# Optimization experiments

Hardware: AMD Instinct MI355X
Metric: run time of the kernel (lower is better)

## Reference

```python
import jax, jax.numpy as jnp
import numpy as np

# Layer widths of the hardcoded torch MLP: 2->128->256->512->512->512->512->256->128->3
_DIMS = [2, 128, 256, 512, 512, 512, 512, 256, 128, 3]


def setup_inputs() -> dict:
    key = jax.random.key(0)
    keys = jax.random.split(key, 2 * (len(_DIMS) - 1) + 1)
    inp = {"x": jax.random.uniform(keys[0], (1048576, 2), dtype=jnp.float32)}
    for i in range(len(_DIMS) - 1):
        fan_in, fan_out = _DIMS[i], _DIMS[i + 1]
        bound = 1.0 / np.sqrt(fan_in)  # torch nn.Linear default init range
        inp[f"W{i+1}"] = jax.random.uniform(keys[2 * i + 1], (fan_in, fan_out), jnp.float32, -bound, bound)
        inp[f"b{i+1}"] = jax.random.uniform(keys[2 * i + 2], (fan_out,), jnp.float32, -bound, bound)
    return inp


def reference(x, W1, b1, W2, b2, W3, b3, W4, b4, W5, b5, W6, b6, W7, b7, W8, b8, W9, b9):
    # (transpose of torch's [out, in]); math is identical: y = x @ W + b.
    h = x
    for W, b in ((W1, b1), (W2, b2), (W3, b3), (W4, b4),
                 (W5, b5), (W6, b6), (W7, b7), (W8, b8)):
        h = jax.nn.relu(h @ W + b)
    return jax.nn.sigmoid(h @ W9 + b9)
```

## Files before the change

kernel.cpp:

```cpp
#include <hip/hip_runtime.h>

typedef _Float16 f16;
typedef __attribute__((ext_vector_type(4))) _Float16 f16x4;
typedef __attribute__((ext_vector_type(8))) _Float16 f16x8;
typedef __attribute__((ext_vector_type(16))) float f32x16;

#define MT 128
#define NBF 4
#define LDSP 1024
#define RING_B 32768

#define OFF2 0
#define OFF3 32768
#define OFF4 163840
#define OFF5 425984
#define OFF6 688128
#define OFF7 950272
#define OFF8 1081344
#define OFF9 1114112
#define TOTAL_FRAG_LANES 139776

__device__ __forceinline__ uint32_t swz(int row, int colbytes) {
  return (uint32_t)(row * LDSP + (colbytes ^ ((row & 31) << 4)));
}

__global__ void repack_kernel(const float* __restrict__ W2, const float* __restrict__ W3,
                              const float* __restrict__ W4, const float* __restrict__ W5,
                              const float* __restrict__ W6, const float* __restrict__ W7,
                              const float* __restrict__ W8, const float* __restrict__ W9,
                              f16* __restrict__ ws) {
  int gid = blockIdx.x * 256 + threadIdx.x;
  if (gid >= TOTAL_FRAG_LANES) return;
  const float* src; int N, NT; size_t dst; int local;
  if      (gid <   4096) { src = W2; N = 256; NT = 8;  dst = OFF2; local = gid;          }
  else if (gid <  20480) { src = W3; N = 512; NT = 16; dst = OFF3; local = gid -   4096; }
  else if (gid <  53248) { src = W4; N = 512; NT = 16; dst = OFF4; local = gid -  20480; }
  else if (gid <  86016) { src = W5; N = 512; NT = 16; dst = OFF5; local = gid -  53248; }
  else if (gid < 118784) { src = W6; N = 512; NT = 16; dst = OFF6; local = gid -  86016; }
  else if (gid < 135168) { src = W7; N = 256; NT = 8;  dst = OFF7; local = gid - 118784; }
  else if (gid < 139264) { src = W8; N = 128; NT = 4;  dst = OFF8; local = gid - 135168; }
  else                   { src = W9; N = 3;   NT = 1;  dst = OFF9; local = gid - 139264; }
  int lane = local & 63;
  int frag = local >> 6;
  int kf = frag / NT, nf = frag % NT;
  int n  = nf * 32 + (lane & 31);
  int kb = kf * 16 + ((lane >> 5) << 3);
  f16x8 v;
  #pragma unroll
  for (int i = 0; i < 8; ++i) {
    float val = (n < N) ? src[(size_t)(kb + i) * N + n] : 0.0f;
    v[i] = (f16)val;
  }
  *reinterpret_cast<f16x8*>(ws + dst + (size_t)local * 8) = v;
}

__device__ __forceinline__ void gload16(const f16* g, char* l) {
  __builtin_amdgcn_global_load_lds(
      (const __attribute__((address_space(1))) void*)g,
      (__attribute__((address_space(3))) void*)l, 16, 0, 0);
}

template<int MF>
__device__ __forceinline__ void stage_step(const f16* __restrict__ wp, int t,
                                           char* ringwave, int wid, int lane) {
  constexpr int KPS = 16 / MF;
  char* dst = ringwave + ((t & 1) << 11);
  int g0, g1;
  if constexpr (MF == 16) { g0 = t * 16 + wid * 2;       g1 = g0 + 1; }
  else                    { g0 = (t * KPS) * MF + wid;   g1 = (t * KPS + 1) * MF + wid; }
  gload16(wp + (size_t)g0 * 512 + (size_t)lane * 8, dst);
  gload16(wp + (size_t)g1 * 512 + (size_t)lane * 8, dst + 1024);
}

template<int KT, int MF, int NXT_MF, bool STAGE_NEXT>
__device__ __forceinline__ void run_staged(char* act, char* ring,
    const f16* __restrict__ wp, const f16* __restrict__ wp_next,
    const float* __restrict__ bias, int tid, f16x8& wc0, f16x8& wc1) {
  constexpr int FM = MF / 8, KPS = 16 / MF, NS = (KT * MF) / 16, BN = KPS * 4;
  const int lane = tid & 63, wid = tid >> 6;
  const int mlane = lane & 31, h = lane >> 5;
  char* ringwave = ring + (wid << 12);
  const uint32_t l16 = (uint32_t)lane * 16;

  f32x16 acc[FM][4];
  #pragma unroll
  for (int fm = 0; fm < FM; ++fm) {
    const int mbase = (wid * FM + fm) * 32;
    #pragma unroll
    for (int g = 0; g < 4; ++g) {
      const float4 bb = *reinterpret_cast<const float4*>(&bias[mbase + g * 8 + 4 * h]);
      #pragma unroll
      for (int j = 0; j < 4; ++j)
        #pragma unroll
        for (int fb = 0; fb < 4; ++fb)
          acc[fm][fb][g * 4 + j] = ((const float*)&bb)[j];
    }
  }

  uint32_t rbase[4], rx[4];
  #pragma unroll
  for (int fb = 0; fb < 4; ++fb) {
    int row = fb * 32 + mlane;
    rbase[fb] = (uint32_t)row * LDSP;
    rx[fb] = (uint32_t)((row & 31) << 4);
  }

  f16x8 cw0 = wc0, cw1 = wc1, nw0, nw1;
  f16x8 cb[BN], nb[BN];
  #pragma unroll
  for (int kk = 0; kk < KPS; ++kk)
    #pragma unroll
    for (int fb = 0; fb < 4; ++fb)
      cb[kk * 4 + fb] = *reinterpret_cast<const f16x8*>(
          act + rbase[fb] + ((uint32_t)(kk * 32 + h * 16) ^ rx[fb]));

#define STEP(S, CW0, CW1, CB, NW0, NW1, NB, DOSTAGE, WAIT0, DOREAD)            \
  {                                                                            \
    asm volatile("s_waitcnt lgkmcnt(0)" ::: "memory");                         \
    if constexpr (DOSTAGE) {                                                   \
      if ((S) + 2 < NS) stage_step<MF>(wp, (S) + 2, ringwave, wid, lane);      \
      else stage_step<NXT_MF>(wp_next, (S) + 2 - NS, ringwave, wid, lane);     \
    }                                                                          \
    __builtin_amdgcn_s_setprio(1);                                             \
    _Pragma("unroll")                                                          \
    for (int fb = 0; fb < 4; ++fb)                                             \
      acc[0][fb] = __builtin_amdgcn_mfma_f32_32x32x16_f16(CW0, CB[fb], acc[0][fb], 0, 0, 0); \
    __builtin_amdgcn_s_setprio(0);                                             \
    if constexpr (WAIT0) { asm volatile("s_waitcnt vmcnt(0)" ::: "memory"); }  \
    else                 { asm volatile("s_waitcnt vmcnt(2)" ::: "memory"); }  \
    if constexpr (DOREAD) {                                                    \
      const char* slot = ringwave + ((((S) + 1) & 1) << 11);                   \
      NW0 = *reinterpret_cast<const f16x8*>(slot + l16);                       \
      NW1 = *reinterpret_cast<const f16x8*>(slot + 1024 + l16);                \
      _Pragma("unroll")                                                        \
      for (int kk = 0; kk < KPS; ++kk)                                         \
        _Pragma("unroll")                                                      \
        for (int fb = 0; fb < 4; ++fb)                                         \
          NB[kk * 4 + fb] = *reinterpret_cast<const f16x8*>(                   \
              act + rbase[fb] + ((uint32_t)((((S) + 1) * KPS + kk) * 32 + h * 16) ^ rx[fb])); \
    }                                                                          \
    __builtin_amdgcn_s_setprio(1);                                             \
    _Pragma("unroll")                                                          \
    for (int fb = 0; fb < 4; ++fb)                                             \
      acc[FM - 1][fb] = __builtin_amdgcn_mfma_f32_32x32x16_f16(CW1, CB[BN - 4 + fb], acc[FM - 1][fb], 0, 0, 0); \
    __builtin_amdgcn_s_setprio(0);                                             \
  }

  constexpr int STEADY = STAGE_NEXT ? NS : NS - 2;
  #pragma unroll 1
  for (int s = 0; s < STEADY; s += 2) {
    STEP(s,     cw0, cw1, cb, nw0, nw1, nb, true, false, true)
    STEP(s + 1, nw0, nw1, nb, cw0, cw1, cb, true, false, true)
  }
  if constexpr (!STAGE_NEXT) {
    STEP(NS - 2, cw0, cw1, cb, nw0, nw1, nb, false, true, true)
    STEP(NS - 1, nw0, nw1, nb, cw0, cw1, cb, false, true, false)
  }
#undef STEP
  wc0 = cw0; wc1 = cw1;

  __syncthreads();
  #pragma unroll
  for (int fm = 0; fm < FM; ++fm) {
    const int mbase = (wid * FM + fm) * 32;
    #pragma unroll
    for (int fb = 0; fb < 4; ++fb) {
      const int row = fb * 32 + mlane;
      #pragma unroll
      for (int g = 0; g < 4; ++g) {
        const int m0 = mbase + g * 8 + 4 * h;
        f16x4 v;
        #pragma unroll
        for (int j = 0; j < 4; ++j)
          v[j] = (f16)fmaxf(acc[fm][fb][g * 4 + j], 0.0f);
        *reinterpret_cast<f16x4*>(act + swz(row, m0 * 2)) = v;
      }
    }
  }
  __syncthreads();
}

template<int KT, int MF, int WMG, int WBG>
__device__ __forceinline__ void run_direct(char* act, const f16* __restrict__ wp,
                                           const float* __restrict__ bias, int tid) {
  constexpr int FM = MF / WMG, FB = NBF / WBG;
  const int lane = tid & 63, wid = tid >> 6;
  const int wm = wid / WBG, wb = wid % WBG;
  const int mlane = lane & 31, h = lane >> 5;

  f32x16 acc[FM][FB];
  #pragma unroll
  for (int fm = 0; fm < FM; ++fm) {
    const int mbase = (wm * FM + fm) * 32;
    #pragma unroll
    for (int g = 0; g < 4; ++g) {
      const float4 bb = *reinterpret_cast<const float4*>(&bias[mbase + g * 8 + 4 * h]);
      #pragma unroll
      for (int j = 0; j < 4; ++j)
        #pragma unroll
        for (int fb = 0; fb < FB; ++fb)
          acc[fm][fb][g * 4 + j] = ((const float*)&bb)[j];
    }
  }
  const f16x8* __restrict__ wfrag = reinterpret_cast<const f16x8*>(wp);
  #pragma unroll 2
  for (int kf = 0; kf < KT; ++kf) {
    f16x8 a[FM];
    #pragma unroll
    for (int fm = 0; fm < FM; ++fm)
      a[fm] = wfrag[(size_t)(kf * MF + wm * FM + fm) * 64 + lane];
    f16x8 b[FB];
    #pragma unroll
    for (int fb = 0; fb < FB; ++fb)
      b[fb] = *reinterpret_cast<const f16x8*>(
          act + swz((wb * FB + fb) * 32 + mlane, kf * 32 + h * 16));
    #pragma unroll
    for (int fm = 0; fm < FM; ++fm)
      #pragma unroll
      for (int fb = 0; fb < FB; ++fb)
        acc[fm][fb] = __builtin_amdgcn_mfma_f32_32x32x16_f16(a[fm], b[fb], acc[fm][fb], 0, 0, 0);
  }
  __syncthreads();
  #pragma unroll
  for (int fm = 0; fm < FM; ++fm) {
    const int mbase = (wm * FM + fm) * 32;
    #pragma unroll
    for (int fb = 0; fb < FB; ++fb) {
      const int row = (wb * FB + fb) * 32 + mlane;
      #pragma unroll
      for (int g = 0; g < 4; ++g) {
        const int m0 = mbase + g * 8 + 4 * h;
        f16x4 v;
        #pragma unroll
        for (int j = 0; j < 4; ++j)
          v[j] = (f16)fmaxf(acc[fm][fb][g * 4 + j], 0.0f);
        *reinterpret_cast<f16x4*>(act + swz(row, m0 * 2)) = v;
      }
    }
  }
  __syncthreads();
}

__global__ __launch_bounds__(512, 2)
void mlp_kernel(const float* __restrict__ x,
                const float* __restrict__ W1, const float* __restrict__ b1,
                const f16*   __restrict__ wpk,
                const float* __restrict__ b2, const float* __restrict__ b3,
                const float* __restrict__ b4, const float* __restrict__ b5,
                const float* __restrict__ b6, const float* __restrict__ b7,
                const float* __restrict__ b8, const float* __restrict__ b9,
                float* __restrict__ out) {
  __shared__ __align__(16) char act[MT * LDSP];
  __shared__ __align__(16) char ring[RING_B];
  const int row0 = blockIdx.x * MT;
  const int tid  = threadIdx.x;
  const int lane = tid & 63, wid = tid >> 6;
  char* ringwave = ring + (wid << 12);

  stage_step<8>(wpk + OFF2, 0, ringwave, wid, lane);
  stage_step<8>(wpk + OFF2, 1, ringwave, wid, lane);

  {
    const int r  = tid >> 2;
    const int cb = (tid & 3) * 32;
    const float2 xv = reinterpret_cast<const float2*>(x)[row0 + r];
    #pragma unroll
    for (int q = 0; q < 4; ++q) {
      f16x8 v;
      #pragma unroll
      for (int j = 0; j < 8; ++j) {
        int c = cb + q * 8 + j;
        v[j] = (f16)fmaxf(fmaf(xv.y, W1[128 + c], fmaf(xv.x, W1[c], b1[c])), 0.0f);
      }
      *reinterpret_cast<f16x8*>(act + swz(r, cb * 2 + q * 16)) = v;
    }
  }
  __syncthreads();

  f16x8 wc0 = *reinterpret_cast<const f16x8*>(ringwave + (uint32_t)lane * 16);
  f16x8 wc1 = *reinterpret_cast<const f16x8*>(ringwave + 1024 + (uint32_t)lane * 16);

  run_staged<8,  8,  16, true >(act, ring, wpk + OFF2, wpk + OFF3, b2, tid, wc0, wc1);
  run_staged<16, 16, 16, true >(act, ring, wpk + OFF3, wpk + OFF4, b3, tid, wc0, wc1);
  #pragma unroll 1
  for (int rep = 0; rep < 2; ++rep)
    run_staged<32, 16, 16, true>(act, ring, wpk + OFF4 + rep * (OFF5 - OFF4),
                                 wpk + OFF5 + rep * (OFF5 - OFF4),
                                 (rep == 0) ? b4 : b5, tid, wc0, wc1);
  run_staged<32, 16, 8,  true >(act, ring, wpk + OFF6, wpk + OFF7, b6, tid, wc0, wc1);
  run_staged<32, 8,  8,  false>(act, ring, wpk + OFF7, wpk,        b7, tid, wc0, wc1);
  run_direct<16, 4, 4, 2>(act, wpk + OFF8, b8, tid);

  if (wid < 4) {
    const int mlane = lane & 31;
    const int h     = lane >> 5;
    f32x16 acc = (f32x16)0.0f;
    const f16x8* __restrict__ wfrag = reinterpret_cast<const f16x8*>(wpk + OFF9);
    #pragma unroll
    for (int kf = 0; kf < 8; ++kf) {
      f16x8 a = wfrag[(size_t)kf * 64 + lane];
      f16x8 b = *reinterpret_cast<const f16x8*>(
          act + swz(wid * 32 + mlane, kf * 32 + h * 16));
      acc = __builtin_amdgcn_mfma_f32_32x32x16_f16(a, b, acc, 0, 0, 0);
    }
    if (h == 0) {
      const size_t orow = (size_t)(row0 + wid * 32 + mlane) * 3;
      #pragma unroll
      for (int r = 0; r < 3; ++r) {
        float v = acc[r] + b9[r];
        out[orow + r] = 1.0f / (1.0f + __expf(-v));
      }
    }
  }
}

extern "C" void kernel_launch(void* const* d_in, const int* in_sizes, int n_in,
                              void* d_out, int out_size, void* d_ws, size_t ws_size,
                              hipStream_t stream) {
  const float* x  = (const float*)d_in[0];
  const float* W1 = (const float*)d_in[1];  const float* b1 = (const float*)d_in[2];
  const float* W2 = (const float*)d_in[3];  const float* b2 = (const float*)d_in[4];
  const float* W3 = (const float*)d_in[5];  const float* b3 = (const float*)d_in[6];
  const float* W4 = (const float*)d_in[7];  const float* b4 = (const float*)d_in[8];
  const float* W5 = (const float*)d_in[9];  const float* b5 = (const float*)d_in[10];
  const float* W6 = (const float*)d_in[11]; const float* b6 = (const float*)d_in[12];
  const float* W7 = (const float*)d_in[13]; const float* b7 = (const float*)d_in[14];
  const float* W8 = (const float*)d_in[15]; const float* b8 = (const float*)d_in[16];
  const float* W9 = (const float*)d_in[17]; const float* b9 = (const float*)d_in[18];
  f16* wpk = (f16*)d_ws;

  repack_kernel<<<(TOTAL_FRAG_LANES + 255) / 256, 256, 0, stream>>>(
      W2, W3, W4, W5, W6, W7, W8, W9, wpk);

  mlp_kernel<<<1048576 / MT, 512, 0, stream>>>(
      x, W1, b1, wpk, b2, b3, b4, b5, b6, b7, b8, b9, (float*)d_out);
}
```

Before: 2.103 ms.

## Replace per-wave double-buffered weight staging with block-shared 4-slot ring

Per-wave 2-slot weight staging is replaced by a block-wide ring of four 8 KB slots, prefetched three chunks ahead with a block barrier each step. For the 512-wide layers the two wave halves take turns on alternate chunks. Each wave now keeps a single chunk of A and B fragments in registers instead of double-buffering them. The aim is deeper prefetch and fewer registers, at the cost of a barrier every chunk and half the waves idling on alternate chunks in the wide layers.

```diff
diff --git a/kernel.cpp b/kernel.cpp
--- a/kernel.cpp
+++ b/kernel.cpp
@@ -8,7 +8,7 @@
 #define MT 128
 #define NBF 4
 #define LDSP 1024
-#define RING_B 32768
+#define SLOT 8192
 
 #define OFF2 0
 #define OFF3 32768
@@ -60,27 +60,22 @@
       (__attribute__((address_space(3))) void*)l, 16, 0, 0);
 }
 
-template<int MF>
-__device__ __forceinline__ void stage_step(const f16* __restrict__ wp, int t,
-                                           char* ringwave, int wid, int lane) {
-  constexpr int KPS = 16 / MF;
-  char* dst = ringwave + ((t & 1) << 11);
-  int g0, g1;
-  if constexpr (MF == 16) { g0 = t * 16 + wid * 2;       g1 = g0 + 1; }
-  else                    { g0 = (t * KPS) * MF + wid;   g1 = (t * KPS + 1) * MF + wid; }
-  gload16(wp + (size_t)g0 * 512 + (size_t)lane * 8, dst);
-  gload16(wp + (size_t)g1 * 512 + (size_t)lane * 8, dst + 1024);
-}
-
-template<int KT, int MF, int NXT_MF, bool STAGE_NEXT>
-__device__ __forceinline__ void run_staged(char* act, char* ring,
+__device__ __forceinline__ void stage8k(const f16* __restrict__ src, char* slotbase, int tid) {
+  const int lane = tid & 63, wid = tid >> 6;
+  gload16(src + (size_t)(wid * 64 + lane) * 8, slotbase + wid * 1024);
+}
+
+template<int KT, int MF>
+__device__ __forceinline__ void run_ring(char* act, char* ring,
     const f16* __restrict__ wp, const f16* __restrict__ wp_next,
-    const float* __restrict__ bias, int tid, f16x8& wc0, f16x8& wc1) {
-  constexpr int FM = MF / 8, KPS = 16 / MF, NS = (KT * MF) / 16, BN = KPS * 4;
+    const float* __restrict__ bias, int tid) {
+  constexpr int NP = KT * MF / 8;
+  constexpr int FM = MF / 8;
   const int lane = tid & 63, wid = tid >> 6;
   const int mlane = lane & 31, h = lane >> 5;
-  char* ringwave = ring + (wid << 12);
+  const int hh = wid >> 2;
   const uint32_t l16 = (uint32_t)lane * 16;
+  const uint32_t woff = (MF == 16) ? (uint32_t)(wid & 3) * 2048 : (uint32_t)wid * 1024;
 
   f32x16 acc[FM][4];
   #pragma unroll
@@ -105,59 +100,57 @@
     rx[fb] = (uint32_t)((row & 31) << 4);
   }
 
-  f16x8 cw0 = wc0, cw1 = wc1, nw0, nw1;
-  f16x8 cb[BN], nb[BN];
-  #pragma unroll
-  for (int kk = 0; kk < KPS; ++kk)
-    #pragma unroll
-    for (int fb = 0; fb < 4; ++fb)
-      cb[kk * 4 + fb] = *reinterpret_cast<const f16x8*>(
-          act + rbase[fb] + ((uint32_t)(kk * 32 + h * 16) ^ rx[fb]));
-
-#define STEP(S, CW0, CW1, CB, NW0, NW1, NB, DOSTAGE, WAIT0, DOREAD)            \
-  {                                                                            \
-    asm volatile("s_waitcnt lgkmcnt(0)" ::: "memory");                         \
-    if constexpr (DOSTAGE) {                                                   \
-      if ((S) + 2 < NS) stage_step<MF>(wp, (S) + 2, ringwave, wid, lane);      \
-      else stage_step<NXT_MF>(wp_next, (S) + 2 - NS, ringwave, wid, lane);     \
-    }                                                                          \
-    __builtin_amdgcn_s_setprio(1);                                             \
-    _Pragma("unroll")                                                          \
-    for (int fb = 0; fb < 4; ++fb)                                             \
-      acc[0][fb] = __builtin_amdgcn_mfma_f32_32x32x16_f16(CW0, CB[fb], acc[0][fb], 0, 0, 0); \
-    __builtin_amdgcn_s_setprio(0);                                             \
-    if constexpr (WAIT0) { asm volatile("s_waitcnt vmcnt(0)" ::: "memory"); }  \
-    else                 { asm volatile("s_waitcnt vmcnt(2)" ::: "memory"); }  \
-    if constexpr (DOREAD) {                                                    \
-      const char* slot = ringwave + ((((S) + 1) & 1) << 11);                   \
-      NW0 = *reinterpret_cast<const f16x8*>(slot + l16);                       \
-      NW1 = *reinterpret_cast<const f16x8*>(slot + 1024 + l16);                \
-      _Pragma("unroll")                                                        \
-      for (int kk = 0; kk < KPS; ++kk)                                         \
-        _Pragma("unroll")                                                      \
-        for (int fb = 0; fb < 4; ++fb)                                         \
-          NB[kk * 4 + fb] = *reinterpret_cast<const f16x8*>(                   \
-              act + rbase[fb] + ((uint32_t)((((S) + 1) * KPS + kk) * 32 + h * 16) ^ rx[fb])); \
-    }                                                                          \
-    __builtin_amdgcn_s_setprio(1);                                             \
-    _Pragma("unroll")                                                          \
-    for (int fb = 0; fb < 4; ++fb)                                             \
-      acc[FM - 1][fb] = __builtin_amdgcn_mfma_f32_32x32x16_f16(CW1, CB[BN - 4 + fb], acc[FM - 1][fb], 0, 0, 0); \
-    __builtin_amdgcn_s_setprio(0);                                             \
-  }
-
-  constexpr int STEADY = STAGE_NEXT ? NS : NS - 2;
+  f16x8 rw0, rw1, rb0, rb1, rb2, rb3;
+#define BREADS(KF)                                                             \
+  rb0 = *reinterpret_cast<const f16x8*>(act + rbase[0] + (((uint32_t)((KF) * 32 + h * 16)) ^ rx[0])); \
+  rb1 = *reinterpret_cast<const f16x8*>(act + rbase[1] + (((uint32_t)((KF) * 32 + h * 16)) ^ rx[1])); \
+  rb2 = *reinterpret_cast<const f16x8*>(act + rbase[2] + (((uint32_t)((KF) * 32 + h * 16)) ^ rx[2])); \
+  rb3 = *reinterpret_cast<const f16x8*>(act + rbase[3] + (((uint32_t)((KF) * 32 + h * 16)) ^ rx[3]))
+
+  {
+    const char* slot = ring + (uint32_t)((MF == 16) ? hh : 0) * SLOT;
+    rw0 = *reinterpret_cast<const f16x8*>(slot + woff + l16);
+    if constexpr (MF == 16)
+      rw1 = *reinterpret_cast<const f16x8*>(slot + woff + 1024 + l16);
+    BREADS(0);
+  }
+
   #pragma unroll 1
-  for (int s = 0; s < STEADY; s += 2) {
-    STEP(s,     cw0, cw1, cb, nw0, nw1, nb, true, false, true)
-    STEP(s + 1, nw0, nw1, nb, cw0, cw1, cb, true, false, true)
-  }
-  if constexpr (!STAGE_NEXT) {
-    STEP(NS - 2, cw0, cw1, cb, nw0, nw1, nb, false, true, true)
-    STEP(NS - 1, nw0, nw1, nb, cw0, cw1, cb, false, true, false)
-  }
-#undef STEP
-  wc0 = cw0; wc1 = cw1;
+  for (int c = 0; c < NP; ++c) {
+    __builtin_amdgcn_s_barrier();
+    const int sc = c + 3;
+    const f16* src = (sc < NP) ? (wp + (size_t)sc * 4096)
+                               : (wp_next + (size_t)(sc - NP) * 4096);
+    stage8k(src, ring + (uint32_t)(sc & 3) * SLOT, tid);
+    asm volatile("s_waitcnt vmcnt(2)" ::: "memory");
+    const bool act_now = (MF == 8) || ((c & 1) == hh);
+    if (act_now) {
+      asm volatile("s_waitcnt lgkmcnt(0)" ::: "memory");
+      __builtin_amdgcn_sched_barrier(0);
+      __builtin_amdgcn_s_setprio(1);
+      acc[0][0] = __builtin_amdgcn_mfma_f32_32x32x16_f16(rw0, rb0, acc[0][0], 0, 0, 0);
+      acc[0][1] = __builtin_amdgcn_mfma_f32_32x32x16_f16(rw0, rb1, acc[0][1], 0, 0, 0);
+      acc[0][2] = __builtin_amdgcn_mfma_f32_32x32x16_f16(rw0, rb2, acc[0][2], 0, 0, 0);
+      acc[0][3] = __builtin_amdgcn_mfma_f32_32x32x16_f16(rw0, rb3, acc[0][3], 0, 0, 0);
+      if constexpr (FM == 2) {
+        acc[1][0] = __builtin_amdgcn_mfma_f32_32x32x16_f16(rw1, rb0, acc[1][0], 0, 0, 0);
+        acc[1][1] = __builtin_amdgcn_mfma_f32_32x32x16_f16(rw1, rb1, acc[1][1], 0, 0, 0);
+        acc[1][2] = __builtin_amdgcn_mfma_f32_32x32x16_f16(rw1, rb2, acc[1][2], 0, 0, 0);
+        acc[1][3] = __builtin_amdgcn_mfma_f32_32x32x16_f16(rw1, rb3, acc[1][3], 0, 0, 0);
+      }
+      __builtin_amdgcn_s_setprio(0);
+    }
+    const int cn = c + 1;
+    if (cn < NP && ((MF == 8) || ((cn & 1) == hh))) {
+      const char* slot = ring + (uint32_t)(cn & 3) * SLOT;
+      const int kfn = (MF == 16) ? (cn >> 1) : cn;
+      rw0 = *reinterpret_cast<const f16x8*>(slot + woff + l16);
+      if constexpr (MF == 16)
+        rw1 = *reinterpret_cast<const f16x8*>(slot + woff + 1024 + l16);
+      BREADS(kfn);
+    }
+  }
+#undef BREADS
 
   __syncthreads();
   #pragma unroll
@@ -187,7 +180,6 @@
   const int lane = tid & 63, wid = tid >> 6;
   const int wm = wid / WBG, wb = wid % WBG;
   const int mlane = lane & 31, h = lane >> 5;
-
   f32x16 acc[FM][FB];
   #pragma unroll
   for (int fm = 0; fm < FM; ++fm) {
@@ -251,14 +243,14 @@
                 const float* __restrict__ b8, const float* __restrict__ b9,
                 float* __restrict__ out) {
   __shared__ __align__(16) char act[MT * LDSP];
-  __shared__ __align__(16) char ring[RING_B];
+  __shared__ __align__(16) char ring[4 * SLOT];
   const int row0 = blockIdx.x * MT;
   const int tid  = threadIdx.x;
   const int lane = tid & 63, wid = tid >> 6;
-  char* ringwave = ring + (wid << 12);
-
-  stage_step<8>(wpk + OFF2, 0, ringwave, wid, lane);
-  stage_step<8>(wpk + OFF2, 1, ringwave, wid, lane);
+
+  stage8k(wpk + OFF2,        ring,            tid);
+  stage8k(wpk + OFF2 + 4096, ring + SLOT,     tid);
+  stage8k(wpk + OFF2 + 8192, ring + 2 * SLOT, tid);
 
   {
     const int r  = tid >> 2;
@@ -277,18 +269,15 @@
   }
   __syncthreads();
 
-  f16x8 wc0 = *reinterpret_cast<const f16x8*>(ringwave + (uint32_t)lane * 16);
-  f16x8 wc1 = *reinterpret_cast<const f16x8*>(ringwave + 1024 + (uint32_t)lane * 16);
-
-  run_staged<8,  8,  16, true >(act, ring, wpk + OFF2, wpk + OFF3, b2, tid, wc0, wc1);
-  run_staged<16, 16, 16, true >(act, ring, wpk + OFF3, wpk + OFF4, b3, tid, wc0, wc1);
+  run_ring<8,  8 >(act, ring, wpk + OFF2, wpk + OFF3, b2, tid);
+  run_ring<16, 16>(act, ring, wpk + OFF3, wpk + OFF4, b3, tid);
   #pragma unroll 1
-  for (int rep = 0; rep < 2; ++rep)
-    run_staged<32, 16, 16, true>(act, ring, wpk + OFF4 + rep * (OFF5 - OFF4),
-                                 wpk + OFF5 + rep * (OFF5 - OFF4),
-                                 (rep == 0) ? b4 : b5, tid, wc0, wc1);
-  run_staged<32, 16, 8,  true >(act, ring, wpk + OFF6, wpk + OFF7, b6, tid, wc0, wc1);
-  run_staged<32, 8,  8,  false>(act, ring, wpk + OFF7, wpk,        b7, tid, wc0, wc1);
+  for (int rep = 0; rep < 3; ++rep) {
+    const float* bias = (rep == 0) ? b4 : (rep == 1) ? b5 : b6;
+    const f16* wp = wpk + OFF4 + rep * (OFF5 - OFF4);
+    run_ring<32, 16>(act, ring, wp, wp + (OFF5 - OFF4), bias, tid);
+  }
+  run_ring<32, 8 >(act, ring, wpk + OFF7, wpk + OFF8, b7, tid);
   run_direct<16, 4, 4, 2>(act, wpk + OFF8, b8, tid);
 
   if (wid < 4) {
```

After: 2.991 ms. 1.42x slower.
